# Performance work log

Measured on AMD Instinct MI355X. Metric: run time of the kernel, lower is better.

## Reference

```python
import jax, jax.numpy as jnp
import numpy as np

N = 100000
E = 1_600_000
C_IN = 128
HID = 64
C_OUT = 64
HEADS = 3
NEG_SLOPE = 0.2  # PyG GATConv default leaky-relu slope


def setup_inputs() -> dict:
    key = jax.random.key(0)
    ks = jax.random.split(key, 8)
    return {
        "node_features": jax.random.normal(ks[0], (N, C_IN), jnp.float32),
        "edge_index": jax.random.randint(ks[1], (2, E), 0, N, jnp.int32),
        "edge_attributes": jax.random.uniform(ks[2], (E,), jnp.float32),
        "W1": jax.random.normal(ks[3], (C_IN, HID), jnp.float32) * 0.1,
        "b1": jnp.zeros((HID,), jnp.float32),
        "W2": jax.random.normal(ks[4], (HID, HEADS * C_OUT), jnp.float32) * 0.1,
        "b2": jnp.zeros((HEADS * C_OUT,), jnp.float32),
        "att_src": jax.random.normal(ks[5], (HEADS, C_OUT), jnp.float32) * 0.1,
        "att_dst": jax.random.normal(ks[6], (HEADS, C_OUT), jnp.float32) * 0.1,
    }


def reference(node_features, edge_index, edge_attributes, W1, b1, W2, b2, att_src, att_dst):
    n = node_features.shape[0]
    loops = jnp.arange(n, dtype=edge_index.dtype)
    # Both GCNConv and GATConv add self-loops by default (fill weight 1.0)
    src = jnp.concatenate([edge_index[0], loops])
    dst = jnp.concatenate([edge_index[1], loops])
    ew = jnp.concatenate([edge_attributes, jnp.ones((n,), node_features.dtype)])

    # ---- GCNConv: symmetric-normalized weighted scatter-add aggregation ----
    deg = jax.ops.segment_sum(ew, dst, num_segments=n)            # [N]
    dis = jnp.where(deg > 0, jax.lax.rsqrt(deg), 0.0)
    norm = dis[src] * ew * dis[dst]                               # [Et]
    xw = node_features @ W1                                       # [N, HID]
    x = jax.ops.segment_sum(xw[src] * norm[:, None], dst, num_segments=n) + b1
    x = jax.nn.relu(x)

    # ---- GATConv (heads concat): per-edge attention + segment softmax ----
    heads, c_out = att_src.shape
    g = (x @ W2).reshape(n, heads, c_out)                          # [N, H, F]
    a_src = jnp.sum(g * att_src, axis=-1)                          # [N, H]
    a_dst = jnp.sum(g * att_dst, axis=-1)                          # [N, H]
    alpha = jax.nn.leaky_relu(a_src[src] + a_dst[dst], NEG_SLOPE)  # [Et, H]
    amax = jax.ops.segment_max(alpha, dst, num_segments=n)         # softmax per dst node
    ex = jnp.exp(alpha - amax[dst])
    denom = jax.ops.segment_sum(ex, dst, num_segments=n)
    attn = ex / (denom[dst] + 1e-16)                               # [Et, H]
    out = jax.ops.segment_sum(g[src] * attn[:, :, None], dst, num_segments=n)
    out = out.reshape(n, heads * c_out) + b2                       # [N, H*F]

    # ---- global_mean_pool(x, None): mean over all nodes -> [1, H*F] ----
    return jnp.mean(out, axis=0, keepdims=True)
```

## Files before the change

### kernel.cpp

```cpp
#include <hip/hip_runtime.h>
#include <hip/hip_fp16.h>
#include <math.h>

typedef unsigned long long u64;
typedef unsigned int u32;

__device__ __forceinline__ float lrelu(float v) { return v > 0.f ? v : 0.2f * v; }
__device__ __forceinline__ u32 fkey(float x) {
    u32 b = __float_as_uint(x);
    return (b & 0x80000000u) ? ~b : (b | 0x80000000u);
}
__device__ __forceinline__ float finv(u32 k) {
    return __uint_as_float((k & 0x80000000u) ? (k & 0x7fffffffu) : ~k);
}

union H2U { __half2 h; u32 u; };


__global__ void k_hist(const int* __restrict__ dst, int* __restrict__ cnt, int E) {
    int e = blockIdx.x * 256 + threadIdx.x;
    if (e < E) atomicAdd(&cnt[dst[e]], 1);
}

__global__ __launch_bounds__(256) void k_scan1(const int* __restrict__ cnt,
                                               int* __restrict__ off,
                                               int* __restrict__ partials, int N) {
    __shared__ int sh[256];
    int tid = threadIdx.x;
    int base = blockIdx.x * 1024 + tid * 4;
    int v[4]; int tsum = 0;
#pragma unroll
    for (int i = 0; i < 4; i++) {
        int n = base + i;
        int c = (n < N) ? cnt[n] + 1 : 0;
        v[i] = tsum; tsum += c;
    }
    sh[tid] = tsum; __syncthreads();
    int mine = tsum;
    for (int o = 1; o < 256; o <<= 1) {
        int t = (tid >= o) ? sh[tid - o] : 0;
        __syncthreads();
        sh[tid] += t;
        __syncthreads();
    }
    int excl = sh[tid] - mine;
#pragma unroll
    for (int i = 0; i < 4; i++) {
        int n = base + i;
        if (n < N) off[n] = excl + v[i];
    }
    if (tid == 255) partials[blockIdx.x] = sh[255];
}

__global__ void k_scan2(int* __restrict__ partials, int nb) {
    __shared__ int sh[256];
    int tid = threadIdx.x;
    int v = (tid < nb) ? partials[tid] : 0;
    sh[tid] = v; __syncthreads();
    for (int o = 1; o < 256; o <<= 1) {
        int t = (tid >= o) ? sh[tid - o] : 0;
        __syncthreads();
        sh[tid] += t;
        __syncthreads();
    }
    if (tid < nb) partials[tid] = sh[tid] - v;
}

__global__ void k_scan3(int* __restrict__ off, int* __restrict__ cursor,
                        const int* __restrict__ partials, int N, int Et) {
    int base = blockIdx.x * 1024 + threadIdx.x * 4;
    int add = partials[blockIdx.x];
#pragma unroll
    for (int i = 0; i < 4; i++) {
        int n = base + i;
        if (n < N) { int o = off[n] + add; off[n] = o; cursor[n] = o; }
    }
    if (blockIdx.x == 0 && threadIdx.x == 0) { off[N] = Et; cursor[N] = Et; }
}

__global__ void k_fill(const int* __restrict__ src, const int* __restrict__ dst,
                       const float* __restrict__ ew, int* __restrict__ cursor,
                       u32* __restrict__ epk, int E, int Et) {
    int e = blockIdx.x * 256 + threadIdx.x;
    if (e >= Et) return;
    int s, d; u32 q;
    if (e < E) {
        s = src[e]; d = dst[e];
        q = min(__float2uint_rn(ew[e] * 32767.f), 32767u);
    } else { s = d = e - E; q = 32767u; }
    int p = atomicAdd(&cursor[d], 1);
    epk[p] = (q << 17) | (u32)s;
}

__global__ void k_degdis(const int* __restrict__ off, const u32* __restrict__ epk,
                         float* __restrict__ dis, int N) {
    int n = blockIdx.x * 256 + threadIdx.x;
    if (n >= N) return;
    int b = off[n], e2 = off[n + 1];
    float s = 0.f;
    for (int i = b; i < e2; i++) s += (float)(epk[i] >> 17);
    dis[n] = rsqrtf(s * (1.f / 32767.f));
}


__global__ __launch_bounds__(256) void k_gemm1(const float* __restrict__ X,
                                               const float* __restrict__ W1,
                                               const float* __restrict__ dis,
                                               __half* __restrict__ xwh, int N) {
    __shared__ __align__(16) float Ws[128 * 64];
    __shared__ __align__(16) float Xs[32][129];
    int tid = threadIdx.x;
    int m0 = blockIdx.x * 32;
    const float4* W4 = (const float4*)W1;
    float4* Ws4 = (float4*)Ws;
#pragma unroll
    for (int i = 0; i < 8; i++) Ws4[tid + i * 256] = W4[tid + i * 256];
#pragma unroll
    for (int i = 0; i < 4; i++) {
        int idx = tid + i * 256;
        int r = idx >> 5;
        int c = idx & 31;
        float4 v = ((const float4*)(X + (size_t)(m0 + r) * 128))[c];
        Xs[r][c * 4 + 0] = v.x; Xs[r][c * 4 + 1] = v.y;
        Xs[r][c * 4 + 2] = v.z; Xs[r][c * 4 + 3] = v.w;
    }
    __syncthreads();
    int r = tid & 31;
    int c0 = (tid >> 5) * 8;
    float acc[8] = {0, 0, 0, 0, 0, 0, 0, 0};
#pragma unroll 4
    for (int k = 0; k < 128; k++) {
        float xv = Xs[r][k];
        const float4* wr = (const float4*)&Ws[k * 64 + c0];
        float4 w0 = wr[0], w1 = wr[1];
        acc[0] += xv * w0.x; acc[1] += xv * w0.y; acc[2] += xv * w0.z; acc[3] += xv * w0.w;
        acc[4] += xv * w1.x; acc[5] += xv * w1.y; acc[6] += xv * w1.z; acc[7] += xv * w1.w;
    }
    float dn = dis[m0 + r];
    H2U p0, p1, p2, p3;
    p0.h = __floats2half2_rn(acc[0] * dn, acc[1] * dn);
    p1.h = __floats2half2_rn(acc[2] * dn, acc[3] * dn);
    p2.h = __floats2half2_rn(acc[4] * dn, acc[5] * dn);
    p3.h = __floats2half2_rn(acc[6] * dn, acc[7] * dn);
    ((uint4*)(xwh + (size_t)(m0 + r) * 64))[c0 >> 3] = make_uint4(p0.u, p1.u, p2.u, p3.u);
}

__global__ __launch_bounds__(256) void k_gcn_agg(const int* __restrict__ off,
                                                 const u32* __restrict__ epk,
                                                 const float* __restrict__ dis,
                                                 const __half* __restrict__ xwh,
                                                 float* __restrict__ x, int N) {
    int lane = threadIdx.x & 63;
    int wv = threadIdx.x >> 6;
    int slot = lane >> 3;
    int f8 = lane & 7;
    int gw = blockIdx.x * 4 + wv;
    int stride = gridDim.x * 4;
    for (int n = gw; n < N; n += stride) {
        int b = off[n], en = off[n + 1];
        float acc[8] = {0, 0, 0, 0, 0, 0, 0, 0};
        for (int c = b; c < en; c += 64) {
            int idx = c + lane;
            int s = 0; float nw = 0.f;
            if (idx < en) {
                u32 pk = epk[idx];
                s = (int)(pk & 0x1FFFFu);
                nw = (float)(pk >> 17) * (1.f / 32767.f);
            }
            int cc = min(64, en - c);
            for (int r = 0; r * 8 < cc; r++) {
                int eo = r * 8 + slot;
                int ss = __shfl(s, eo);
                float nn = __shfl(nw, eo);
                if (eo < cc) {
                    uint4 raw = ((const uint4*)(xwh + (size_t)ss * 64))[f8];
                    __half2* hp = (__half2*)&raw;
                    float2 q0 = __half22float2(hp[0]);
                    float2 q1 = __half22float2(hp[1]);
                    float2 q2 = __half22float2(hp[2]);
                    float2 q3 = __half22float2(hp[3]);
                    acc[0] += nn * q0.x; acc[1] += nn * q0.y;
                    acc[2] += nn * q1.x; acc[3] += nn * q1.y;
                    acc[4] += nn * q2.x; acc[5] += nn * q2.y;
                    acc[6] += nn * q3.x; acc[7] += nn * q3.y;
                }
            }
        }
#pragma unroll
        for (int j = 0; j < 8; j++) {
            acc[j] += __shfl_xor(acc[j], 8);
            acc[j] += __shfl_xor(acc[j], 16);
            acc[j] += __shfl_xor(acc[j], 32);
        }
        if (lane < 8) {
            float dn = dis[n];
            ((float4*)(x + (size_t)n * 64))[f8 * 2 + 0] =
                make_float4(acc[0] * dn, acc[1] * dn, acc[2] * dn, acc[3] * dn);
            ((float4*)(x + (size_t)n * 64))[f8 * 2 + 1] =
                make_float4(acc[4] * dn, acc[5] * dn, acc[6] * dn, acc[7] * dn);
        }
    }
}

__global__ __launch_bounds__(256) void k_gemm2(const float* __restrict__ x,
                                               const float* __restrict__ W2,
                                               const float* __restrict__ b1,
                                               const float* __restrict__ att_src,
                                               const float* __restrict__ att_dst,
                                               __half* __restrict__ gh,
                                               float* __restrict__ asrc4,
                                               float* __restrict__ adst4,
                                               u32* __restrict__ amaxk, int N) {
    __shared__ __align__(16) float Ws[64 * 192];
    __shared__ __align__(16) float Xs[32][65];
    __shared__ float b1s[64];
    __shared__ float as_s[192], ad_s[192];
    int tid = threadIdx.x;
    int m0 = blockIdx.x * 32;
    if (tid < 64) b1s[tid] = b1[tid];
    if (tid < 192) { as_s[tid] = att_src[tid]; ad_s[tid] = att_dst[tid]; }
    __syncthreads();
    const float4* W4 = (const float4*)W2;
    float4* Ws4 = (float4*)Ws;
#pragma unroll
    for (int i = 0; i < 12; i++) Ws4[tid + i * 256] = W4[tid + i * 256];
#pragma unroll
    for (int i = 0; i < 2; i++) {
        int idx = tid + i * 256;
        int r = idx >> 4;
        int c4 = idx & 15;
        float4 v = ((const float4*)(x + (size_t)(m0 + r) * 64))[c4];
        v.x = fmaxf(v.x + b1s[c4 * 4 + 0], 0.f);
        v.y = fmaxf(v.y + b1s[c4 * 4 + 1], 0.f);
        v.z = fmaxf(v.z + b1s[c4 * 4 + 2], 0.f);
        v.w = fmaxf(v.w + b1s[c4 * 4 + 3], 0.f);
        Xs[r][c4 * 4 + 0] = v.x; Xs[r][c4 * 4 + 1] = v.y;
        Xs[r][c4 * 4 + 2] = v.z; Xs[r][c4 * 4 + 3] = v.w;
    }
    __syncthreads();
    int r = tid & 31;
    int c0 = (tid >> 5) * 24;
    float acc[24];
#pragma unroll
    for (int j = 0; j < 24; j++) acc[j] = 0.f;
#pragma unroll 4
    for (int k = 0; k < 64; k++) {
        float xv = Xs[r][k];
        const float4* wr = (const float4*)&Ws[k * 192 + c0];
#pragma unroll
        for (int q = 0; q < 6; q++) {
            float4 wv = wr[q];
            acc[q * 4 + 0] += xv * wv.x;
            acc[q * 4 + 1] += xv * wv.y;
            acc[q * 4 + 2] += xv * wv.z;
            acc[q * 4 + 3] += xv * wv.w;
        }
    }
    __half* outp = gh + (size_t)(m0 + r) * 192 + c0;
#pragma unroll
    for (int t = 0; t < 3; t++) {
        H2U p0, p1, p2, p3;
        p0.h = __floats2half2_rn(acc[t * 8 + 0], acc[t * 8 + 1]);
        p1.h = __floats2half2_rn(acc[t * 8 + 2], acc[t * 8 + 3]);
        p2.h = __floats2half2_rn(acc[t * 8 + 4], acc[t * 8 + 5]);
        p3.h = __floats2half2_rn(acc[t * 8 + 6], acc[t * 8 + 7]);
        ((uint4*)outp)[t] = make_uint4(p0.u, p1.u, p2.u, p3.u);
    }

    float sa0 = 0.f, sa1 = 0.f, sb0 = 0.f, sb1 = 0.f;
    int h0 = c0 >> 6;
    int split = 64 - (c0 & 63); if (split > 24) split = 24;
#pragma unroll
    for (int j = 0; j < 24; j++) {
        float va = acc[j] * as_s[c0 + j];
        float vb = acc[j] * ad_s[c0 + j];
        if (j < split) { sa0 += va; sb0 += vb; }
        else           { sa1 += va; sb1 += vb; }
    }
    __syncthreads();
    float* S = &Xs[0][0];
    for (int i = tid; i < 1536; i += 256) S[i] = 0.f;
    __syncthreads();
    int ct = tid >> 5;
    int slot = (r * 8 + ct) * 3;
    S[slot + h0] = sa0;
    S[768 + slot + h0] = sb0;
    if (split < 24) { S[slot + h0 + 1] = sa1; S[768 + slot + h0 + 1] = sb1; }
    __syncthreads();
    if (tid < 96) {
        int rr = tid / 3, h = tid - 3 * rr;
        float sA = 0.f, sB = 0.f;
#pragma unroll
        for (int c = 0; c < 8; c++) {
            sA += S[(rr * 8 + c) * 3 + h];
            sB += S[768 + (rr * 8 + c) * 3 + h];
        }
        asrc4[(size_t)(m0 + rr) * 4 + h] = sA;
        adst4[(size_t)(m0 + rr) * 4 + h] = sB;
        S[1536 + tid] = sA;
    }
    __syncthreads();
    if (tid < 3) {
        float m = -1e30f;
        for (int rr = 0; rr < 32; rr++) m = fmaxf(m, S[1536 + rr * 3 + tid]);
        atomicMax(&amaxk[tid], fkey(m));
    }
}

__global__ __launch_bounds__(256) void k_gatsm(const int* __restrict__ off,
                                               const u32* __restrict__ epk,
                                               const float* __restrict__ asrc4,
                                               const float* __restrict__ adst4,
                                               const u32* __restrict__ amaxk,
                                               u64* __restrict__ wpk, int N) {
    int n = blockIdx.x * 256 + threadIdx.x;
    if (n >= N) return;
    int b = off[n], en = off[n + 1];
    float4 ad = ((const float4*)adst4)[n];
    float M0 = lrelu(finv(amaxk[0]) + ad.x);
    float M1 = lrelu(finv(amaxk[1]) + ad.y);
    float M2 = lrelu(finv(amaxk[2]) + ad.z);
    float s0 = 0.f, s1 = 0.f, s2 = 0.f;
    for (int i = b; i < en; i++) {
        int s = (int)(epk[i] & 0x1FFFFu);
        float4 av = ((const float4*)asrc4)[s];
        s0 += __expf(lrelu(av.x + ad.x) - M0);
        s1 += __expf(lrelu(av.y + ad.y) - M1);
        s2 += __expf(lrelu(av.z + ad.z) - M2);
    }
    float i0 = 8192.f / (s0 + 1e-16f);
    float i1 = 8192.f / (s1 + 1e-16f);
    float i2 = 8192.f / (s2 + 1e-16f);
    for (int i = b; i < en; i++) {
        int s = (int)(epk[i] & 0x1FFFFu);
        float4 av = ((const float4*)asrc4)[s];
        u32 q0 = __float2uint_rn(__expf(lrelu(av.x + ad.x) - M0) * i0);
        u32 q1 = __float2uint_rn(__expf(lrelu(av.y + ad.y) - M1) * i1);
        u32 q2 = __float2uint_rn(__expf(lrelu(av.z + ad.z) - M2) * i2);
        u64 pk = (u64)q0 | ((u64)q1 << 21) | ((u64)q2 << 42);
        atomicAdd(&wpk[s], pk);
    }
}

__global__ __launch_bounds__(192) void k_wsum(const u64* __restrict__ wpk,
                                              const __half* __restrict__ gh,
                                              float* __restrict__ gsum, int N) {
    int j = threadIdx.x;
    int sh = 21 * (j >> 6);
    int gs = gridDim.x;
    float a = 0.f;
    for (int n = blockIdx.x; n < N; n += gs) {
        u64 pk = wpk[n];
        float wn = (float)((u32)(pk >> sh) & 0x1FFFFFu);
        a += wn * __half2float(gh[(size_t)n * 192 + j]);
    }
    atomicAdd(&gsum[j], a);
}

__global__ void k_final(const float* __restrict__ gsum, const float* __restrict__ b2,
                        float* __restrict__ out, float inv) {
    int j = threadIdx.x;
    if (j < 192) out[j] = gsum[j] * inv + b2[j];
}

extern "C" void kernel_launch(void* const* d_in, const int* in_sizes, int n_in,
                              void* d_out, int out_size, void* d_ws, size_t ws_size,
                              hipStream_t stream) {
    const float* X   = (const float*)d_in[0];
    const int*   ei  = (const int*)d_in[1];
    const float* ew  = (const float*)d_in[2];
    const float* W1  = (const float*)d_in[3];
    const float* b1  = (const float*)d_in[4];
    const float* W2  = (const float*)d_in[5];
    const float* b2  = (const float*)d_in[6];
    const float* ats = (const float*)d_in[7];
    const float* atd = (const float*)d_in[8];

    int N  = in_sizes[0] / 128;
    int E  = in_sizes[1] / 2;
    int Et = E + N;
    const int* srcI = ei;
    const int* dstI = ei + E;

    float* ws = (float*)d_ws;
    int*   wsi = (int*)d_ws;

    size_t o = 0;
    int* off_p = wsi + o;           o += (size_t)N + 1;
    int* cur_p = wsi + o;           o += (size_t)N + 1;
    o = (o + 1) & ~(size_t)1;
    size_t z0 = o;
    u64* wpk   = (u64*)(wsi + o);   o += (size_t)N * 2;
    int* cnt_p = wsi + o;           o += (size_t)N;
    float* gsum = ws + o;           o += 192;
    u32* amaxk = (u32*)(wsi + o);   o += 4;
    size_t z1 = o;
    int* part_p = wsi + o;          o += 256;
    float* dis  = ws + o;           o += (size_t)N;
    o = (o + 3) & ~(size_t)3;
    float* asrc4 = ws + o;          o += (size_t)N * 4;
    float* adst4 = ws + o;          o += (size_t)N * 4;
    float* x     = ws + o;          o += (size_t)N * 64;
    __half* xwh  = (__half*)(ws + o); o += (size_t)N * 32;
    __half* gh   = (__half*)(ws + o); o += (size_t)N * 96;
    u32* epk = (u32*)(ws + o);

    hipMemsetAsync(wsi + z0, 0, (z1 - z0) * sizeof(int), stream);

    int nb = (N + 1023) / 1024;

    k_hist <<<(E + 255) / 256, 256, 0, stream>>>(dstI, cnt_p, E);
    k_scan1<<<nb, 256, 0, stream>>>(cnt_p, off_p, part_p, N);
    k_scan2<<<1, 256, 0, stream>>>(part_p, nb);
    k_scan3<<<nb, 256, 0, stream>>>(off_p, cur_p, part_p, N, Et);
    k_fill <<<(Et + 255) / 256, 256, 0, stream>>>(srcI, dstI, ew, cur_p, epk, E, Et);
    k_degdis<<<(N + 255) / 256, 256, 0, stream>>>(off_p, epk, dis, N);
    k_gemm1<<<N / 32, 256, 0, stream>>>(X, W1, dis, xwh, N);
    k_gcn_agg<<<2048, 256, 0, stream>>>(off_p, epk, dis, xwh, x, N);
    k_gemm2<<<N / 32, 256, 0, stream>>>(x, W2, b1, ats, atd, gh, asrc4, adst4, amaxk, N);
    k_gatsm<<<(N + 255) / 256, 256, 0, stream>>>(off_p, epk, asrc4, adst4, amaxk, wpk, N);
    k_wsum<<<512, 192, 0, stream>>>(wpk, gh, gsum, N);
    k_final<<<1, 192, 0, stream>>>(gsum, b2, (float*)d_out, 1.0f / (8192.0f * (float)N));
}
```

Before: 612.2 us.

## Partition histogram and CSR fill atomics into eight destination ranges per block group

The histogram and CSR fill kernels now use a fixed grid of grid-stride blocks split into eight groups. Each group scans all edges but only does atomics for destinations in its eighth of the node range. The aim is to keep each group's atomic targets in a smaller, more cache- or XCD-local slice of memory, so scattered atomics contend less. The cost is that every edge's dst is read eight times, which adds read traffic and extra branching.

```diff
diff --git a/kernel.cpp b/kernel.cpp
--- a/kernel.cpp
+++ b/kernel.cpp
@@ -17,9 +17,17 @@
 union H2U { __half2 h; u32 u; };
 
 
-__global__ void k_hist(const int* __restrict__ dst, int* __restrict__ cnt, int E) {
-    int e = blockIdx.x * 256 + threadIdx.x;
-    if (e < E) atomicAdd(&cnt[dst[e]], 1);
+__global__ __launch_bounds__(256) void k_hist(const int* __restrict__ dst,
+                                              int* __restrict__ cnt, int E, int N) {
+    int p = blockIdx.x & 7;
+    int lo = (int)((long long)p * N / 8);
+    int hi = (int)((long long)(p + 1) * N / 8);
+    int bi = blockIdx.x >> 3;
+    int nb = gridDim.x >> 3;
+    for (int e = bi * 256 + threadIdx.x; e < E; e += nb * 256) {
+        int d = dst[e];
+        if (d >= lo && d < hi) atomicAdd(&cnt[d], 1);
+    }
 }
 
 __global__ __launch_bounds__(256) void k_scan1(const int* __restrict__ cnt,
@@ -78,18 +86,28 @@
     if (blockIdx.x == 0 && threadIdx.x == 0) { off[N] = Et; cursor[N] = Et; }
 }
 
-__global__ void k_fill(const int* __restrict__ src, const int* __restrict__ dst,
-                       const float* __restrict__ ew, int* __restrict__ cursor,
-                       u32* __restrict__ epk, int E, int Et) {
-    int e = blockIdx.x * 256 + threadIdx.x;
-    if (e >= Et) return;
-    int s, d; u32 q;
-    if (e < E) {
-        s = src[e]; d = dst[e];
-        q = min(__float2uint_rn(ew[e] * 32767.f), 32767u);
-    } else { s = d = e - E; q = 32767u; }
-    int p = atomicAdd(&cursor[d], 1);
-    epk[p] = (q << 17) | (u32)s;
+__global__ __launch_bounds__(256) void k_fill(const int* __restrict__ src,
+                                              const int* __restrict__ dst,
+                                              const float* __restrict__ ew,
+                                              int* __restrict__ cursor,
+                                              u32* __restrict__ epk,
+                                              int E, int Et, int N) {
+    int p = blockIdx.x & 7;
+    int lo = (int)((long long)p * N / 8);
+    int hi = (int)((long long)(p + 1) * N / 8);
+    int bi = blockIdx.x >> 3;
+    int nb = gridDim.x >> 3;
+    for (int e = bi * 256 + threadIdx.x; e < Et; e += nb * 256) {
+        int d = (e < E) ? dst[e] : e - E;
+        if (d < lo || d >= hi) continue;
+        int s; u32 q;
+        if (e < E) {
+            s = src[e];
+            q = min(__float2uint_rn(ew[e] * 32767.f), 32767u);
+        } else { s = d; q = 32767u; }
+        int pos = atomicAdd(&cursor[d], 1);
+        epk[pos] = (q << 17) | (u32)s;
+    }
 }
 
 __global__ void k_degdis(const int* __restrict__ off, const u32* __restrict__ epk,
@@ -409,11 +427,11 @@
 
     int nb = (N + 1023) / 1024;
 
-    k_hist <<<(E + 255) / 256, 256, 0, stream>>>(dstI, cnt_p, E);
+    k_hist <<<2048, 256, 0, stream>>>(dstI, cnt_p, E, N);
     k_scan1<<<nb, 256, 0, stream>>>(cnt_p, off_p, part_p, N);
     k_scan2<<<1, 256, 0, stream>>>(part_p, nb);
     k_scan3<<<nb, 256, 0, stream>>>(off_p, cur_p, part_p, N, Et);
-    k_fill <<<(Et + 255) / 256, 256, 0, stream>>>(srcI, dstI, ew, cur_p, epk, E, Et);
+    k_fill <<<2048, 256, 0, stream>>>(srcI, dstI, ew, cur_p, epk, E, Et, N);
     k_degdis<<<(N + 255) / 256, 256, 0, stream>>>(off_p, epk, dis, N);
     k_gemm1<<<N / 32, 256, 0, stream>>>(X, W1, dis, xwh, N);
     k_gcn_agg<<<2048, 256, 0, stream>>>(off_p, epk, dis, xwh, x, N);
```

Result: faster. 574.2 us (-6.2%).
